# Kernel optimization log

Hardware: AMD Instinct MI355X
Metric: run time of the kernel (lower is better)

The kernel has to match this reference:

```python
import jax, jax.numpy as jnp
import numpy as np

N_USERS, N_ITEMS, D = 16384, 8192, 64
IMG_D, TXT_D = 4096, 384
TOPK = 10
LAMBDA = 0.9         # args.lambda_coeff
NNZ = 786432
N_TOTAL = N_USERS + N_ITEMS


def l2norm(x, eps=1e-12):
    # F.normalize(p=2, dim=1)
    return x / jnp.maximum(jnp.linalg.norm(x, axis=-1, keepdims=True), eps)


def build_knn_graph(feats):
    """build_sim + build_knn_normalized_graph (sparse, sym norm).
    Returns row-sparse KNN graph as (values [N,k], indices [N,k])."""
    z = l2norm(feats)
    sim = z @ z.T                          # [N, N] cosine similarity
    vals, inds = jax.lax.top_k(sim, TOPK)  # [N, k]
    rowsum = vals.sum(axis=1)              # degree
    d_inv_sqrt = jnp.where(rowsum > 0, rowsum, 1.0) ** -0.5
    vals = vals * d_inv_sqrt[:, None] * d_inv_sqrt[inds]  # D^-1/2 A D^-1/2
    return vals, inds


def knn_mm(vals, inds, x):
    # sparse.mm with row-sparse [N,k] graph: out[i] = sum_k vals[i,k]*x[inds[i,k]]
    return jnp.einsum('nk,nkd->nd', vals, x[inds])


def setup_inputs() -> dict:
    key = jax.random.key(0)
    ks = jax.random.split(key, 16)
    xav = lambda k, shp: jax.random.normal(k, shp, jnp.float32) * (2.0 / (shp[0] + shp[-1])) ** 0.5
    return dict(
        adj_rows=jax.random.randint(ks[0], (NNZ,), 0, N_TOTAL, jnp.int32),
        adj_cols=jax.random.randint(ks[1], (NNZ,), 0, N_TOTAL, jnp.int32),
        adj_vals=jax.random.uniform(ks[2], (NNZ,), jnp.float32) / 32.0,
        image_feats=jax.random.normal(ks[3], (N_ITEMS, IMG_D), jnp.float32),
        text_feats=jax.random.normal(ks[4], (N_ITEMS, TXT_D), jnp.float32),
        user_emb=xav(ks[5], (N_USERS, D)),
        item_emb=xav(ks[6], (N_ITEMS, D)),
        img_w=xav(ks[7], (IMG_D, D)), img_b=jnp.zeros((D,), jnp.float32),
        txt_w=xav(ks[8], (TXT_D, D)), txt_b=jnp.zeros((D,), jnp.float32),
        q_w1=xav(ks[9], (D, D)), q_b1=jnp.zeros((D,), jnp.float32),
        q_w2=xav(ks[10], (D, 1)),
        gc_w=xav(ks[11], (2, D, D)), gc_b=jnp.zeros((2, D), jnp.float32),
        bi_w=xav(ks[12], (2, D, D)), bi_b=jnp.zeros((2, D), jnp.float32),
    )


def reference(adj_rows, adj_cols, adj_vals, image_feats, text_feats,
              user_emb, item_emb, img_w, img_b, txt_w, txt_b,
              q_w1, q_b1, q_w2, gc_w, gc_b, bi_w, bi_b):
    # original (init-time) modal graphs from raw features
    io_v, io_i = build_knn_graph(image_feats)
    to_v, to_i = build_knn_graph(text_feats)
    # projected modal features + dynamic graphs (build_item_graph=True)
    img_f = image_feats @ img_w + img_b
    txt_f = text_feats @ txt_w + txt_b
    in_v, in_i = build_knn_graph(img_f)
    tn_v, tn_i = build_knn_graph(txt_f)
    # one propagation layer over (1-l)*new_adj + l*orig_adj (separable for layers=1)
    e = item_emb
    img_e = (1 - LAMBDA) * knn_mm(in_v, in_i, e) + LAMBDA * knn_mm(io_v, io_i, e)
    txt_e = (1 - LAMBDA) * knn_mm(tn_v, tn_i, e) + LAMBDA * knn_mm(to_v, to_i, e)
    # attention-weighted fusion
    query = lambda x: jnp.tanh(x @ q_w1 + q_b1) @ q_w2   # [N_ITEMS, 1]
    att = jnp.concatenate([query(img_e), query(txt_e)], axis=-1)
    w = jax.nn.softmax(att, axis=-1)
    h = w[:, :1] * img_e + w[:, 1:] * txt_e
    # NGCF user-item propagation (dropout p=0 -> identity)
    ego = jnp.concatenate([user_emb, item_emb], axis=0)   # [N_TOTAL, D]
    all_e = [ego]
    for i in range(2):
        side = jax.ops.segment_sum(adj_vals[:, None] * ego[adj_cols], adj_rows,
                                   num_segments=N_TOTAL)
        s = jax.nn.leaky_relu(side @ gc_w[i] + gc_b[i])
        b = jax.nn.leaky_relu((ego * side) @ bi_w[i] + bi_b[i])
        ego = s + b
        all_e.append(l2norm(ego))
    all_e = jnp.mean(jnp.stack(all_e, axis=1), axis=1)
    u_g, i_g = all_e[:N_USERS], all_e[N_USERS:]
    i_g = i_g + l2norm(h)
    return u_g, i_g, img_e, txt_e, h
```

## Files before the change

### kernel.cpp

```cpp
#include <hip/hip_runtime.h>
#include <hip/hip_bf16.h>
#include <math.h>

#define N_USERS 16384
#define N_ITEMS 8192
#define N_TOTAL 24576
#define EMB_D 64
#define IMG_DIM 4096
#define TXT_DIM 384
#define K_TOP 10
#define N_CAND 16
#define NNZ_E 786432

typedef _Float16 f16x8 __attribute__((ext_vector_type(8)));
typedef float f32x4 __attribute__((ext_vector_type(4)));

#define AS1 __attribute__((address_space(1)))
#define AS3 __attribute__((address_space(3)))

__device__ __forceinline__ float leaky01(float x){ return x >= 0.f ? x : 0.01f * x; }

__device__ __forceinline__ void gld16(const void* g, void* l) {
  __builtin_amdgcn_global_load_lds((const AS1 unsigned int*)g, (AS3 unsigned int*)l, 16, 0, 0);
}

__device__ __forceinline__ bool beats(float v, int i, float u, int j) {
  return v > u || (v == u && i < j);
}

__device__ __forceinline__ float h2f(unsigned short u) {
  _Float16 h = __builtin_bit_cast(_Float16, u);
  return (float)h;
}

__global__ __launch_bounds__(256) void norm_cast_fused_k(const float* __restrict__ x,
                                                         float* __restrict__ invn,
                                                         unsigned short* __restrict__ zh, int K) {
  __shared__ __align__(16) float xr[4096];
  __shared__ float red[256];
  int r = blockIdx.x;
  const float* xp = x + (size_t)r * K;
  float ss = 0.f;
  for (int j = threadIdx.x; j < K; j += 256) { float v = xp[j]; xr[j] = v; ss += v * v; }
  red[threadIdx.x] = ss; __syncthreads();
  for (int s = 128; s > 0; s >>= 1) {
    if (threadIdx.x < s) red[threadIdx.x] += red[threadIdx.x + s];
    __syncthreads();
  }
  float inv = 1.f / fmaxf(sqrtf(red[0]), 1e-12f);
  if (threadIdx.x == 0) invn[r] = inv;
  for (int j = threadIdx.x; j < K; j += 256) {
    _Float16 h = (_Float16)(xr[j] * inv);
    zh[(size_t)r * K + j] = __builtin_bit_cast(unsigned short, h);
  }
}

#define EPI_LD 136
__global__ __launch_bounds__(256) void sim_mfma_k(const unsigned short* __restrict__ Zh,
                                                  unsigned short* __restrict__ C, int K, int r0) {
  __shared__ __align__(16) unsigned short smem[128 * EPI_LD];
  unsigned short* smA = smem;
  unsigned short* smB = smem + 128 * 32;
  const int tid = threadIdx.x;
  const int lane = tid & 63;
  const int wid = tid >> 6;
  const int wr = wid >> 1, wc = wid & 1;
  const int bRow = r0 + blockIdx.y * 128;
  const int bCol = blockIdx.x * 128;

  f32x4 acc[4][4];
  const f32x4 fzero = {0.f, 0.f, 0.f, 0.f};
  #pragma unroll
  for (int m = 0; m < 4; m++)
    #pragma unroll
    for (int n = 0; n < 4; n++) acc[m][n] = fzero;

  const int u0 = (wid * 2 + 0) * 64 + lane;
  const int u1 = (wid * 2 + 1) * 64 + lane;
  const int ar0 = u0 >> 2, ac0 = (u0 & 3) * 8;
  const int ar1 = u1 >> 2, ac1 = (u1 & 3) * 8;
  const size_t rowA0 = (size_t)(bRow + ar0) * K;
  const size_t rowA1 = (size_t)(bRow + ar1) * K;
  const size_t rowB0 = (size_t)(bCol + ar0) * K;
  const size_t rowB1 = (size_t)(bCol + ar1) * K;
  unsigned short* ldsA0 = smA + (wid * 2 + 0) * 512;
  unsigned short* ldsA1 = smA + (wid * 2 + 1) * 512;
  unsigned short* ldsB0 = smB + (wid * 2 + 0) * 512;
  unsigned short* ldsB1 = smB + (wid * 2 + 1) * 512;

  const int kc = lane >> 4;
  const int fr = lane & 15;

  for (int k0 = 0; k0 < K; k0 += 32) {
    __syncthreads();
    gld16(Zh + rowA0 + k0 + ac0, ldsA0);
    gld16(Zh + rowA1 + k0 + ac1, ldsA1);
    gld16(Zh + rowB0 + k0 + ac0, ldsB0);
    gld16(Zh + rowB1 + k0 + ac1, ldsB1);
    __syncthreads();

    f16x8 a[4], b[4];
    #pragma unroll
    for (int m = 0; m < 4; m++)
      a[m] = *(const f16x8*)&smA[(wr * 64 + m * 16 + fr) * 32 + kc * 8];
    #pragma unroll
    for (int n = 0; n < 4; n++)
      b[n] = *(const f16x8*)&smB[(wc * 64 + n * 16 + fr) * 32 + kc * 8];
    #pragma unroll
    for (int m = 0; m < 4; m++)
      #pragma unroll
      for (int n = 0; n < 4; n++)
        acc[m][n] = __builtin_amdgcn_mfma_f32_16x16x32_f16(a[m], b[n], acc[m][n], 0, 0, 0);
  }

  __syncthreads();
  const int lr = wr * 64 + (lane >> 4) * 4;
  const int lc = wc * 64 + (lane & 15);
  #pragma unroll
  for (int m = 0; m < 4; m++)
    #pragma unroll
    for (int n = 0; n < 4; n++)
      #pragma unroll
      for (int r = 0; r < 4; r++) {
        _Float16 hv = (_Float16)acc[m][n][r];
        smem[(lr + m * 16 + r) * EPI_LD + lc + n * 16] = __builtin_bit_cast(unsigned short, hv);
      }
  __syncthreads();
  const int outRow0 = blockIdx.y * 128;
  #pragma unroll
  for (int i = 0; i < 8; i++) {
    int idx = i * 2048 + tid * 8;
    int rr = idx >> 7, cc = idx & 127;
    *(uint4*)&C[(size_t)(outRow0 + rr) * N_ITEMS + bCol + cc] =
        *(const uint4*)&smem[rr * EPI_LD + cc];
  }
}

__device__ __forceinline__ void ins4(float val, int idx, float tv[4], int ti[4]) {
  if (beats(val, idx, tv[3], ti[3])) {
    tv[3] = val; ti[3] = idx;
    if (beats(tv[3], ti[3], tv[2], ti[2])) { float a=tv[2];int b=ti[2]; tv[2]=tv[3];ti[2]=ti[3]; tv[3]=a;ti[3]=b; }
    if (beats(tv[2], ti[2], tv[1], ti[1])) { float a=tv[1];int b=ti[1]; tv[1]=tv[2];ti[1]=ti[2]; tv[2]=a;ti[2]=b; }
    if (beats(tv[1], ti[1], tv[0], ti[0])) { float a=tv[0];int b=ti[0]; tv[0]=tv[1];ti[0]=ti[1]; tv[1]=a;ti[1]=b; }
  }
}

__global__ __launch_bounds__(256) void topk16h_k(const unsigned short* __restrict__ sim,
                                                 int r0, int* __restrict__ cand) {
  int row = blockIdx.x * 4 + (threadIdx.x >> 6);
  int lane = threadIdx.x & 63;
  const uint4* s8 = reinterpret_cast<const uint4*>(sim + (size_t)row * N_ITEMS);

  float tv[4]; int ti[4];
  #pragma unroll
  for (int k = 0; k < 4; k++) { tv[k] = -INFINITY; ti[k] = 0x7fffffff; }
  unsigned long long ext0 = 0ull, ext1 = 0ull;

  for (int i = 0; i < 16; i++) {
    uint4 v = s8[i * 64 + lane];
    int base = (i * 64 + lane) * 8;
    ins4(h2f(v.x & 0xffff), base + 0, tv, ti);
    ins4(h2f(v.x >> 16),    base + 1, tv, ti);
    ins4(h2f(v.y & 0xffff), base + 2, tv, ti);
    ins4(h2f(v.y >> 16),    base + 3, tv, ti);
    ins4(h2f(v.z & 0xffff), base + 4, tv, ti);
    ins4(h2f(v.z >> 16),    base + 5, tv, ti);
    ins4(h2f(v.w & 0xffff), base + 6, tv, ti);
    ins4(h2f(v.w >> 16),    base + 7, tv, ti);
  }
  int nvalid = 4;
  for (int t = 0; t < N_CAND; t++) {
    float bv = tv[0]; int bi = ti[0];
    for (int o = 32; o; o >>= 1) {
      float ov = __shfl_xor(bv, o, 64);
      int   oi = __shfl_xor(bi, o, 64);
      if (beats(ov, oi, bv, bi)) { bv = ov; bi = oi; }
    }
    if (tv[0] == bv && ti[0] == bi) {
      int slot = ((bi >> 9) << 3) | (bi & 7);
      if (slot < 64) ext0 |= 1ull << slot; else ext1 |= 1ull << (slot - 64);
      tv[0]=tv[1];ti[0]=ti[1]; tv[1]=tv[2];ti[1]=ti[2]; tv[2]=tv[3];ti[2]=ti[3];
      tv[3]=-INFINITY; ti[3]=0x7fffffff;
      nvalid--;
      if (nvalid == 0) {
        for (int i = 0; i < 16; i++) {
          uint4 v = s8[i * 64 + lane];
          int base = (i * 64 + lane) * 8;
          float vv[8] = {h2f(v.x & 0xffff), h2f(v.x >> 16), h2f(v.y & 0xffff), h2f(v.y >> 16),
                         h2f(v.z & 0xffff), h2f(v.z >> 16), h2f(v.w & 0xffff), h2f(v.w >> 16)};
          #pragma unroll
          for (int q = 0; q < 8; q++) {
            int slot2 = i * 8 + q;
            bool used = (slot2 < 64) ? ((ext0 >> slot2) & 1ull) : ((ext1 >> (slot2 - 64)) & 1ull);
            if (!used) ins4(vv[q], base + q, tv, ti);
          }
        }
        nvalid = 4;
      }
    }
    if (lane == 0) cand[(size_t)(r0 + row) * N_CAND + t] = bi;
  }
}

__global__ __launch_bounds__(256) void refine_k(const float* __restrict__ X, int K,
                                                const float* __restrict__ invn,
                                                const int* __restrict__ cand,
                                                float* __restrict__ vals, int* __restrict__ inds,
                                                float* __restrict__ dis) {
  __shared__ __align__(16) float xr[4096];
  __shared__ float dots[N_CAND];
  int row = blockIdx.x;
  int tid = threadIdx.x, lane = tid & 63, wid = tid >> 6;
  for (int j = tid; j < K; j += 256) xr[j] = X[(size_t)row * K + j];
  __syncthreads();
  for (int c = wid; c < N_CAND; c += 4) {
    int ci = cand[(size_t)row * N_CAND + c];
    const float* xc = X + (size_t)ci * K;
    float p = 0.f;
    if (K == 4096) {
      const float4* xc4 = reinterpret_cast<const float4*>(xc);
      const float4* xr4 = reinterpret_cast<const float4*>(xr);
      for (int it = 0; it < 16; it++) {
        float4 a = xr4[it * 64 + lane];
        float4 g = xc4[it * 64 + lane];
        p += a.x * g.x + a.y * g.y + a.z * g.z + a.w * g.w;
      }
    } else {
      for (int j = lane; j < K; j += 64) p += xr[j] * xc[j];
    }
    for (int o = 32; o; o >>= 1) p += __shfl_xor(p, o, 64);
    if (lane == 0) dots[c] = p;
  }
  __syncthreads();
  if (tid == 0) {
    float v[N_CAND]; int id[N_CAND];
    float ir = invn[row];
    for (int c = 0; c < N_CAND; c++) {
      id[c] = cand[(size_t)row * N_CAND + c];
      v[c] = dots[c] * ir * invn[id[c]];
    }
    for (int a = 1; a < N_CAND; a++) {
      float av = v[a]; int ai = id[a];
      int b = a - 1;
      while (b >= 0 && beats(av, ai, v[b], id[b])) { v[b+1]=v[b]; id[b+1]=id[b]; b--; }
      v[b+1] = av; id[b+1] = ai;
    }
    float sum = 0.f;
    for (int t = 0; t < K_TOP; t++) {
      vals[(size_t)row * K_TOP + t] = v[t];
      inds[(size_t)row * K_TOP + t] = id[t];
      sum += v[t];
    }
    float rs = sum > 0.f ? sum : 1.0f;
    dis[row] = 1.0f / sqrtf(rs);
  }
}

__global__ __launch_bounds__(256) void scale_vals_k(float* __restrict__ vals,
                                                    const int* __restrict__ inds,
                                                    const float* __restrict__ dis, int tot) {
  int idx = blockIdx.x * 256 + threadIdx.x;
  if (idx < tot) {
    int i = idx / K_TOP;
    vals[idx] *= dis[i] * dis[inds[idx]];
  }
}

__global__ __launch_bounds__(256) void linear_splitk_k(const float* __restrict__ X,
                                                       const float* __restrict__ W,
                                                       const float* __restrict__ b,
                                                       float* __restrict__ outp, int K, int KS) {
  __shared__ float As[64][17];
  __shared__ float Ws[16][64];
  int br = blockIdx.x, ks = blockIdx.y;
  int tid = threadIdx.x, tr = tid >> 4, tc = tid & 15;
  int k0 = ks * KS, k1 = k0 + KS;
  int lrow = tid >> 2, lk = (tid & 3) * 4;
  int wrow = tid >> 4, wcol = (tid & 15) * 4;
  float acc[4][4] = {};
  for (int kb = k0; kb < k1; kb += 16) {
    __syncthreads();
    float4 xv = *(const float4*)&X[(size_t)(br * 64 + lrow) * K + kb + lk];
    As[lrow][lk + 0] = xv.x; As[lrow][lk + 1] = xv.y;
    As[lrow][lk + 2] = xv.z; As[lrow][lk + 3] = xv.w;
    *(float4*)&Ws[wrow][wcol] = *(const float4*)&W[(size_t)(kb + wrow) * 64 + wcol];
    __syncthreads();
    #pragma unroll
    for (int k = 0; k < 16; k++) {
      float a[4], w[4];
      #pragma unroll
      for (int i = 0; i < 4; i++) a[i] = As[tr * 4 + i][k];
      #pragma unroll
      for (int j = 0; j < 4; j++) w[j] = Ws[k][tc * 4 + j];
      #pragma unroll
      for (int i = 0; i < 4; i++)
        #pragma unroll
        for (int j = 0; j < 4; j++) acc[i][j] += a[i] * w[j];
    }
  }
  #pragma unroll
  for (int i = 0; i < 4; i++)
    #pragma unroll
    for (int j = 0; j < 4; j++) {
      float v = acc[i][j];
      if (ks == 0) v += b[tc * 4 + j];
      atomicAdd(&outp[(size_t)(br * 64 + tr * 4 + i) * 64 + tc * 4 + j], v);
    }
}

__global__ __launch_bounds__(256) void fuse_knn_k(const float* __restrict__ av, const int* __restrict__ ai,
                                                  const float* __restrict__ bv, const int* __restrict__ bi_,
                                                  const float* __restrict__ e, float* __restrict__ outp,
                                                  float lam) {
  int i = blockIdx.x * 4 + (threadIdx.x >> 6), d = threadIdx.x & 63;
  float sa = 0.f, sb = 0.f;
  #pragma unroll
  for (int k = 0; k < K_TOP; k++) {
    sa += av[(size_t)i * K_TOP + k] * e[(size_t)ai[(size_t)i * K_TOP + k] * 64 + d];
    sb += bv[(size_t)i * K_TOP + k] * e[(size_t)bi_[(size_t)i * K_TOP + k] * 64 + d];
  }
  outp[(size_t)i * 64 + d] = (1.f - lam) * sa + lam * sb;
}

__global__ __launch_bounds__(64) void attn_k(const float* __restrict__ img_e, const float* __restrict__ txt_e,
                                             const float* __restrict__ qw1, const float* __restrict__ qb1,
                                             const float* __restrict__ qw2, float* __restrict__ h) {
  __shared__ float W1[64][64];
  __shared__ float sI[64], sT[64];
  int t = threadIdx.x; int i = blockIdx.x;
  for (int k = 0; k < 64; k++) W1[k][t] = qw1[k * 64 + t];
  sI[t] = img_e[(size_t)i * 64 + t];
  sT[t] = txt_e[(size_t)i * 64 + t];
  __syncthreads();
  float yi = qb1[t], yt = qb1[t];
  #pragma unroll 16
  for (int k = 0; k < 64; k++) { yi += sI[k] * W1[k][t]; yt += sT[k] * W1[k][t]; }
  float w2 = qw2[t];
  float pi = tanhf(yi) * w2, pt = tanhf(yt) * w2;
  for (int o = 32; o > 0; o >>= 1) { pi += __shfl_xor(pi, o, 64); pt += __shfl_xor(pt, o, 64); }
  float m = fmaxf(pi, pt);
  float ei = expf(pi - m), et = expf(pt - m);
  float den = ei + et;
  float w0 = ei / den, w1v = et / den;
  h[(size_t)i * 64 + t] = w0 * sI[t] + w1v * sT[t];
}

__global__ __launch_bounds__(256) void hist_k(const int* __restrict__ rows, int* __restrict__ cnt) {
  int e = blockIdx.x * 256 + threadIdx.x;
  if (e < NNZ_E) atomicAdd(&cnt[rows[e]], 1);
}

__global__ __launch_bounds__(256) void scan_k(const int* __restrict__ cnt,
                                              int* __restrict__ starts,
                                              int* __restrict__ cursor) {
  __shared__ int part[256];
  int t = threadIdx.x;
  int base = t * (N_TOTAL / 256);
  int s = 0;
  for (int j = 0; j < N_TOTAL / 256; j++) s += cnt[base + j];
  part[t] = s;
  __syncthreads();
  for (int off = 1; off < 256; off <<= 1) {
    int v = part[t];
    int u = (t >= off) ? part[t - off] : 0;
    __syncthreads();
    part[t] = v + u;
    __syncthreads();
  }
  int run = (t > 0) ? part[t - 1] : 0;
  for (int j = 0; j < N_TOTAL / 256; j++) {
    starts[base + j] = run;
    cursor[base + j] = run;
    run += cnt[base + j];
  }
  if (t == 255) starts[N_TOTAL] = run;
}

__global__ __launch_bounds__(256) void place_k(const int* __restrict__ rows,
                                               int* __restrict__ cursor, int* __restrict__ perm) {
  int e = blockIdx.x * 256 + threadIdx.x;
  if (e < NNZ_E) {
    int p = atomicAdd(&cursor[rows[e]], 1);
    perm[p] = e;
  }
}

__global__ __launch_bounds__(256) void gather_gcn_k(const int* __restrict__ starts,
                                                    const int* __restrict__ perm,
                                                    const int* __restrict__ cols,
                                                    const float* __restrict__ vals,
                                                    const float* __restrict__ ego,
                                                    float* __restrict__ side) {
  int row = blockIdx.x * 4 + (threadIdx.x >> 6);
  int d = threadIdx.x & 63;
  int s = starts[row], e = starts[row + 1];
  float acc = 0.f;
  for (int i = s; i < e; i++) {
    int eid = perm[i];
    acc += vals[eid] * ego[(size_t)cols[eid] * 64 + d];
  }
  side[(size_t)row * 64 + d] = acc;
}

__global__ __launch_bounds__(256) void gcn_k(const float* __restrict__ side, const float* __restrict__ ego,
                                             const float* __restrict__ gw, const float* __restrict__ gb,
                                             const float* __restrict__ bw, const float* __restrict__ bb,
                                             float* __restrict__ outp) {
  __shared__ float W1[64][64], W2[64][64];
  __shared__ float S[4][64], E[4][64];
  int t = threadIdx.x & 63, rb = threadIdx.x >> 6;
  int r = blockIdx.x * 4 + rb;
  for (int idx = threadIdx.x; idx < 4096; idx += 256) {
    W1[idx >> 6][idx & 63] = gw[idx];
    W2[idx >> 6][idx & 63] = bw[idx];
  }
  S[rb][t] = side[(size_t)r * 64 + t];
  E[rb][t] = ego[(size_t)r * 64 + t];
  __syncthreads();
  float s = gb[t], b = bb[t];
  #pragma unroll 16
  for (int k = 0; k < 64; k++) {
    float sv = S[rb][k];
    s += sv * W1[k][t];
    b += E[rb][k] * sv * W2[k][t];
  }
  outp[(size_t)r * 64 + t] = leaky01(s) + leaky01(b);
}

__global__ __launch_bounds__(256) void l2acc_k(const float* __restrict__ ego, float* __restrict__ acc) {
  int r = blockIdx.x * 4 + (threadIdx.x >> 6), d = threadIdx.x & 63;
  float v = ego[(size_t)r * 64 + d];
  float ss = v * v;
  for (int o = 32; o > 0; o >>= 1) ss += __shfl_xor(ss, o, 64);
  float inv = 1.f / fmaxf(sqrtf(ss), 1e-12f);
  acc[(size_t)r * 64 + d] += v * inv;
}

__global__ __launch_bounds__(256) void init_ego_k(const float* __restrict__ ue, const float* __restrict__ ie,
                                                  float* __restrict__ ego, float* __restrict__ acc) {
  int r = blockIdx.x * 4 + (threadIdx.x >> 6), d = threadIdx.x & 63;
  float v = (r < N_USERS) ? ue[(size_t)r * 64 + d] : ie[(size_t)(r - N_USERS) * 64 + d];
  ego[(size_t)r * 64 + d] = v;
  acc[(size_t)r * 64 + d] = v;
}

__global__ __launch_bounds__(256) void final_k(const float* __restrict__ acc, const float* __restrict__ h,
                                               float* __restrict__ u_g, float* __restrict__ i_g) {
  int r = blockIdx.x * 4 + (threadIdx.x >> 6), d = threadIdx.x & 63;
  float m = acc[(size_t)r * 64 + d] * (1.0f / 3.0f);
  if (r < N_USERS) {
    u_g[(size_t)r * 64 + d] = m;
  } else {
    int i = r - N_USERS;
    float hv = h[(size_t)i * 64 + d];
    float ss = hv * hv;
    for (int o = 32; o > 0; o >>= 1) ss += __shfl_xor(ss, o, 64);
    float inv = 1.f / fmaxf(sqrtf(ss), 1e-12f);
    i_g[(size_t)i * 64 + d] = m + hv * inv;
  }
}

static void build_graph(hipStream_t stream, const float* feats, int K, float* invn,
                        unsigned short* zh, unsigned short* sim, int stripe, int* cand,
                        float* vals, int* inds, float* dis) {
  norm_cast_fused_k<<<N_ITEMS, 256, 0, stream>>>(feats, invn, zh, K);
  for (int r0 = 0; r0 < N_ITEMS; r0 += stripe) {
    int rows = (N_ITEMS - r0) < stripe ? (N_ITEMS - r0) : stripe;
    dim3 g(N_ITEMS / 128, rows / 128);
    sim_mfma_k<<<g, 256, 0, stream>>>(zh, sim, K, r0);
    topk16h_k<<<rows / 4, 256, 0, stream>>>(sim, r0, cand);
  }
  refine_k<<<N_ITEMS, 256, 0, stream>>>(feats, K, invn, cand, vals, inds, dis);
  int tot = N_ITEMS * K_TOP;
  scale_vals_k<<<(tot + 255) / 256, 256, 0, stream>>>(vals, inds, dis, tot);
}

extern "C" void kernel_launch(void* const* d_in, const int* in_sizes, int n_in,
                              void* d_out, int out_size, void* d_ws, size_t ws_size,
                              hipStream_t stream) {
  const int*   adj_rows   = (const int*)d_in[0];
  const int*   adj_cols   = (const int*)d_in[1];
  const float* adj_vals   = (const float*)d_in[2];
  const float* image_feats= (const float*)d_in[3];
  const float* text_feats = (const float*)d_in[4];
  const float* user_emb   = (const float*)d_in[5];
  const float* item_emb   = (const float*)d_in[6];
  const float* img_w      = (const float*)d_in[7];
  const float* img_b      = (const float*)d_in[8];
  const float* txt_w      = (const float*)d_in[9];
  const float* txt_b      = (const float*)d_in[10];
  const float* q_w1       = (const float*)d_in[11];
  const float* q_b1       = (const float*)d_in[12];
  const float* q_w2       = (const float*)d_in[13];
  const float* gc_w       = (const float*)d_in[14];
  const float* gc_b       = (const float*)d_in[15];
  const float* bi_w       = (const float*)d_in[16];
  const float* bi_b       = (const float*)d_in[17];

  float* out  = (float*)d_out;
  float* u_g  = out;
  float* i_g  = u_g + (size_t)N_USERS * 64;
  float* imgE = i_g + (size_t)N_ITEMS * 64;
  float* txtE = imgE + (size_t)N_ITEMS * 64;
  float* hOut = txtE + (size_t)N_ITEMS * 64;

  float* W = (float*)d_ws;
  size_t off = 0;
  auto alloc = [&](size_t n) { float* q = W + off; off += n; return q; };
  float* inv_io = alloc(N_ITEMS);
  float* inv_to = alloc(N_ITEMS);
  float* inv_in = alloc(N_ITEMS);
  float* inv_tn = alloc(N_ITEMS);
  float* img_f  = alloc((size_t)N_ITEMS * 64);
  float* txt_f  = alloc((size_t)N_ITEMS * 64);
  float* vals0 = alloc(N_ITEMS * K_TOP); int* inds0 = (int*)alloc(N_ITEMS * K_TOP);
  float* vals1 = alloc(N_ITEMS * K_TOP); int* inds1 = (int*)alloc(N_ITEMS * K_TOP);
  float* vals2 = alloc(N_ITEMS * K_TOP); int* inds2 = (int*)alloc(N_ITEMS * K_TOP);
  float* vals3 = alloc(N_ITEMS * K_TOP); int* inds3 = (int*)alloc(N_ITEMS * K_TOP);
  float* dis0 = alloc(N_ITEMS);
  float* dis1 = alloc(N_ITEMS);
  float* dis2 = alloc(N_ITEMS);
  float* dis3 = alloc(N_ITEMS);
  int*   cand = (int*)alloc((size_t)N_ITEMS * N_CAND);
  float* ego_a = alloc((size_t)N_TOTAL * 64);
  float* ego_b = alloc((size_t)N_TOTAL * 64);
  float* side  = alloc((size_t)N_TOTAL * 64);
  float* acc   = alloc((size_t)N_TOTAL * 64);
  int* csr_cnt    = (int*)alloc(N_TOTAL);
  int* csr_starts = (int*)alloc(N_TOTAL + 1);
  int* csr_cursor = (int*)alloc(N_TOTAL);
  int* csr_perm   = (int*)alloc(NNZ_E);
  unsigned short* zh = (unsigned short*)alloc(((size_t)N_ITEMS * IMG_DIM) / 2);
  unsigned short* sim = (unsigned short*)(W + off);

  size_t used_bytes = off * 4;
  size_t avail_b = (ws_size > used_bytes) ? (ws_size - used_bytes) : 0;
  long stripe_l = (long)((avail_b / ((size_t)N_ITEMS * 2)) / 128) * 128;
  if (stripe_l > N_ITEMS) stripe_l = N_ITEMS;
  if (stripe_l < 128) stripe_l = 128;
  int stripe = (int)stripe_l;

  hipMemsetAsync(csr_cnt, 0, N_TOTAL * sizeof(int), stream);
  hist_k<<<(NNZ_E + 255) / 256, 256, 0, stream>>>(adj_rows, csr_cnt);
  scan_k<<<1, 256, 0, stream>>>(csr_cnt, csr_starts, csr_cursor);
  place_k<<<(NNZ_E + 255) / 256, 256, 0, stream>>>(adj_rows, csr_cursor, csr_perm);

  build_graph(stream, image_feats, IMG_DIM, inv_io, zh, sim, stripe, cand, vals0, inds0, dis0);
  build_graph(stream, text_feats,  TXT_DIM, inv_to, zh, sim, stripe, cand, vals1, inds1, dis1);

  hipMemsetAsync(img_f, 0, (size_t)N_ITEMS * 64 * sizeof(float), stream);
  hipMemsetAsync(txt_f, 0, (size_t)N_ITEMS * 64 * sizeof(float), stream);
  linear_splitk_k<<<dim3(N_ITEMS / 64, 4), 256, 0, stream>>>(image_feats, img_w, img_b, img_f, IMG_DIM, IMG_DIM / 4);
  linear_splitk_k<<<dim3(N_ITEMS / 64, 4), 256, 0, stream>>>(text_feats,  txt_w, txt_b, txt_f, TXT_DIM, TXT_DIM / 4);

  build_graph(stream, img_f, 64, inv_in, zh, sim, stripe, cand, vals2, inds2, dis2);
  build_graph(stream, txt_f, 64, inv_tn, zh, sim, stripe, cand, vals3, inds3, dis3);

  const float lam = 0.9f;
  fuse_knn_k<<<N_ITEMS / 4, 256, 0, stream>>>(vals2, inds2, vals0, inds0, item_emb, imgE, lam);
  fuse_knn_k<<<N_ITEMS / 4, 256, 0, stream>>>(vals3, inds3, vals1, inds1, item_emb, txtE, lam);

  attn_k<<<N_ITEMS, 64, 0, stream>>>(imgE, txtE, q_w1, q_b1, q_w2, hOut);

  init_ego_k<<<N_TOTAL / 4, 256, 0, stream>>>(user_emb, item_emb, ego_a, acc);

  gather_gcn_k<<<N_TOTAL / 4, 256, 0, stream>>>(csr_starts, csr_perm, adj_cols, adj_vals, ego_a, side);
  gcn_k<<<N_TOTAL / 4, 256, 0, stream>>>(side, ego_a, gc_w, gc_b, bi_w, bi_b, ego_b);
  l2acc_k<<<N_TOTAL / 4, 256, 0, stream>>>(ego_b, acc);

  gather_gcn_k<<<N_TOTAL / 4, 256, 0, stream>>>(csr_starts, csr_perm, adj_cols, adj_vals, ego_b, side);
  gcn_k<<<N_TOTAL / 4, 256, 0, stream>>>(side, ego_b, gc_w + 4096, gc_b + 64, bi_w + 4096, bi_b + 64, ego_a);
  l2acc_k<<<N_TOTAL / 4, 256, 0, stream>>>(ego_a, acc);

  final_k<<<N_TOTAL / 4, 256, 0, stream>>>(acc, hOut, u_g, i_g);
}
```

Baseline: 2.847 ms.

## Exploit similarity symmetry with triangular tiles and store sim matrix in fp32

When the full similarity matrix fits in workspace, the GEMM launches only upper-triangular tiles and writes each off-diagonal tile twice (direct and transposed), which about halves the MFMA work. The sim buffer changes from fp16 to fp32, and top-k reads float4 instead of unpacking halves. In exchange, the sim write and read traffic doubles, the transposed stores are strided and uncoalesced, and a smaller stripe fits in the workspace, which may push execution onto the striped fallback path.

Measured after the change: 2.797 ms. No clear change (-1.8%).

```diff
diff --git a/kernel.cpp b/kernel.cpp
--- a/kernel.cpp
+++ b/kernel.cpp
@@ -11,6 +11,8 @@
 #define K_TOP 10
 #define N_CAND 16
 #define NNZ_E 786432
+#define NTILE 64
+#define TRI_BLOCKS (NTILE * (NTILE + 1) / 2)
 
 typedef _Float16 f16x8 __attribute__((ext_vector_type(8)));
 typedef float f32x4 __attribute__((ext_vector_type(4)));
@@ -26,11 +28,6 @@
 
 __device__ __forceinline__ bool beats(float v, int i, float u, int j) {
   return v > u || (v == u && i < j);
-}
-
-__device__ __forceinline__ float h2f(unsigned short u) {
-  _Float16 h = __builtin_bit_cast(_Float16, u);
-  return (float)h;
 }
 
 __global__ __launch_bounds__(256) void norm_cast_fused_k(const float* __restrict__ x,
@@ -55,18 +52,26 @@
   }
 }
 
-#define EPI_LD 136
 __global__ __launch_bounds__(256) void sim_mfma_k(const unsigned short* __restrict__ Zh,
-                                                  unsigned short* __restrict__ C, int K, int r0) {
-  __shared__ __align__(16) unsigned short smem[128 * EPI_LD];
-  unsigned short* smA = smem;
-  unsigned short* smB = smem + 128 * 32;
+                                                  float* __restrict__ C, int K, int r0, int tri) {
+  __shared__ unsigned short smA[128 * 32];
+  __shared__ unsigned short smB[128 * 32];
   const int tid = threadIdx.x;
   const int lane = tid & 63;
   const int wid = tid >> 6;
   const int wr = wid >> 1, wc = wid & 1;
-  const int bRow = r0 + blockIdx.y * 128;
-  const int bCol = blockIdx.x * 128;
+
+  int tileX, tileY;
+  if (tri) {
+    int b = blockIdx.x, ty = 0, rem = NTILE;
+    while (b >= rem) { b -= rem; ty++; rem--; }
+    tileY = ty; tileX = ty + b;
+  } else {
+    tileX = blockIdx.x; tileY = blockIdx.y;
+  }
+
+  const int bRow = r0 + tileY * 128;
+  const int bCol = tileX * 128;
 
   f32x4 acc[4][4];
   const f32x4 fzero = {0.f, 0.f, 0.f, 0.f};
@@ -113,26 +118,22 @@
         acc[m][n] = __builtin_amdgcn_mfma_f32_16x16x32_f16(a[m], b[n], acc[m][n], 0, 0, 0);
   }
 
-  __syncthreads();
-  const int lr = wr * 64 + (lane >> 4) * 4;
-  const int lc = wc * 64 + (lane & 15);
+  const int crow = tileY * 128 + wr * 64 + (lane >> 4) * 4;
+  const int ccol = bCol + wc * 64 + (lane & 15);
   #pragma unroll
   for (int m = 0; m < 4; m++)
     #pragma unroll
     for (int n = 0; n < 4; n++)
       #pragma unroll
-      for (int r = 0; r < 4; r++) {
-        _Float16 hv = (_Float16)acc[m][n][r];
-        smem[(lr + m * 16 + r) * EPI_LD + lc + n * 16] = __builtin_bit_cast(unsigned short, hv);
-      }
-  __syncthreads();
-  const int outRow0 = blockIdx.y * 128;
-  #pragma unroll
-  for (int i = 0; i < 8; i++) {
-    int idx = i * 2048 + tid * 8;
-    int rr = idx >> 7, cc = idx & 127;
-    *(uint4*)&C[(size_t)(outRow0 + rr) * N_ITEMS + bCol + cc] =
-        *(const uint4*)&smem[rr * EPI_LD + cc];
+      for (int r = 0; r < 4; r++)
+        C[(size_t)(crow + m * 16 + r) * N_ITEMS + ccol + n * 16] = acc[m][n][r];
+
+  if (tri && tileX != tileY) {
+    #pragma unroll
+    for (int m = 0; m < 4; m++)
+      #pragma unroll
+      for (int n = 0; n < 4; n++)
+        *(f32x4*)&C[(size_t)(ccol + n * 16) * N_ITEMS + crow + m * 16] = acc[m][n];
   }
 }
 
@@ -145,28 +146,24 @@
   }
 }
 
-__global__ __launch_bounds__(256) void topk16h_k(const unsigned short* __restrict__ sim,
-                                                 int r0, int* __restrict__ cand) {
+__global__ __launch_bounds__(256) void topk16_k(const float* __restrict__ sim,
+                                                int r0, int* __restrict__ cand) {
   int row = blockIdx.x * 4 + (threadIdx.x >> 6);
   int lane = threadIdx.x & 63;
-  const uint4* s8 = reinterpret_cast<const uint4*>(sim + (size_t)row * N_ITEMS);
+  const float4* s4 = reinterpret_cast<const float4*>(sim + (size_t)row * N_ITEMS);
 
   float tv[4]; int ti[4];
   #pragma unroll
   for (int k = 0; k < 4; k++) { tv[k] = -INFINITY; ti[k] = 0x7fffffff; }
   unsigned long long ext0 = 0ull, ext1 = 0ull;
 
-  for (int i = 0; i < 16; i++) {
-    uint4 v = s8[i * 64 + lane];
-    int base = (i * 64 + lane) * 8;
-    ins4(h2f(v.x & 0xffff), base + 0, tv, ti);
-    ins4(h2f(v.x >> 16),    base + 1, tv, ti);
-    ins4(h2f(v.y & 0xffff), base + 2, tv, ti);
-    ins4(h2f(v.y >> 16),    base + 3, tv, ti);
-    ins4(h2f(v.z & 0xffff), base + 4, tv, ti);
-    ins4(h2f(v.z >> 16),    base + 5, tv, ti);
-    ins4(h2f(v.w & 0xffff), base + 6, tv, ti);
-    ins4(h2f(v.w >> 16),    base + 7, tv, ti);
+  for (int i = 0; i < 32; i++) {
+    float4 v = s4[i * 64 + lane];
+    int base = (i * 64 + lane) * 4;
+    ins4(v.x, base + 0, tv, ti);
+    ins4(v.y, base + 1, tv, ti);
+    ins4(v.z, base + 2, tv, ti);
+    ins4(v.w, base + 3, tv, ti);
   }
   int nvalid = 4;
   for (int t = 0; t < N_CAND; t++) {
@@ -177,20 +174,19 @@
       if (beats(ov, oi, bv, bi)) { bv = ov; bi = oi; }
     }
     if (tv[0] == bv && ti[0] == bi) {
-      int slot = ((bi >> 9) << 3) | (bi & 7);
+      int slot = ((bi >> 8) << 2) | (bi & 3);
       if (slot < 64) ext0 |= 1ull << slot; else ext1 |= 1ull << (slot - 64);
       tv[0]=tv[1];ti[0]=ti[1]; tv[1]=tv[2];ti[1]=ti[2]; tv[2]=tv[3];ti[2]=ti[3];
       tv[3]=-INFINITY; ti[3]=0x7fffffff;
       nvalid--;
       if (nvalid == 0) {
-        for (int i = 0; i < 16; i++) {
-          uint4 v = s8[i * 64 + lane];
-          int base = (i * 64 + lane) * 8;
-          float vv[8] = {h2f(v.x & 0xffff), h2f(v.x >> 16), h2f(v.y & 0xffff), h2f(v.y >> 16),
-                         h2f(v.z & 0xffff), h2f(v.z >> 16), h2f(v.w & 0xffff), h2f(v.w >> 16)};
+        for (int i = 0; i < 32; i++) {
+          float4 v = s4[i * 64 + lane];
+          int base = (i * 64 + lane) * 4;
+          float vv[4] = {v.x, v.y, v.z, v.w};
           #pragma unroll
-          for (int q = 0; q < 8; q++) {
-            int slot2 = i * 8 + q;
+          for (int q = 0; q < 4; q++) {
+            int slot2 = i * 4 + q;
             bool used = (slot2 < 64) ? ((ext0 >> slot2) & 1ull) : ((ext1 >> (slot2 - 64)) & 1ull);
             if (!used) ins4(vv[q], base + q, tv, ti);
           }
@@ -461,14 +457,19 @@
 }
 
 static void build_graph(hipStream_t stream, const float* feats, int K, float* invn,
-                        unsigned short* zh, unsigned short* sim, int stripe, int* cand,
+                        unsigned short* zh, float* sim, int stripe, int* cand,
                         float* vals, int* inds, float* dis) {
   norm_cast_fused_k<<<N_ITEMS, 256, 0, stream>>>(feats, invn, zh, K);
-  for (int r0 = 0; r0 < N_ITEMS; r0 += stripe) {
-    int rows = (N_ITEMS - r0) < stripe ? (N_ITEMS - r0) : stripe;
-    dim3 g(N_ITEMS / 128, rows / 128);
-    sim_mfma_k<<<g, 256, 0, stream>>>(zh, sim, K, r0);
-    topk16h_k<<<rows / 4, 256, 0, stream>>>(sim, r0, cand);
+  if (stripe >= N_ITEMS) {
+    sim_mfma_k<<<TRI_BLOCKS, 256, 0, stream>>>(zh, sim, K, 0, 1);
+    topk16_k<<<N_ITEMS / 4, 256, 0, stream>>>(sim, 0, cand);
+  } else {
+    for (int r0 = 0; r0 < N_ITEMS; r0 += stripe) {
+      int rows = (N_ITEMS - r0) < stripe ? (N_ITEMS - r0) : stripe;
+      dim3 g(N_ITEMS / 128, rows / 128);
+      sim_mfma_k<<<g, 256, 0, stream>>>(zh, sim, K, r0, 0);
+      topk16_k<<<rows / 4, 256, 0, stream>>>(sim, r0, cand);
+    }
   }
   refine_k<<<N_ITEMS, 256, 0, stream>>>(feats, K, invn, cand, vals, inds, dis);
   int tot = N_ITEMS * K_TOP;
@@ -531,11 +532,11 @@
   int* csr_cursor = (int*)alloc(N_TOTAL);
   int* csr_perm   = (int*)alloc(NNZ_E);
   unsigned short* zh = (unsigned short*)alloc(((size_t)N_ITEMS * IMG_DIM) / 2);
-  unsigned short* sim = (unsigned short*)(W + off);
-
-  size_t used_bytes = off * 4;
-  size_t avail_b = (ws_size > used_bytes) ? (ws_size - used_bytes) : 0;
-  long stripe_l = (long)((avail_b / ((size_t)N_ITEMS * 2)) / 128) * 128;
+  float* sim = W + off;
+
+  size_t ws_floats = ws_size / 4;
+  size_t avail = (ws_floats > off) ? (ws_floats - off) : 0;
+  long stripe_l = (long)((avail / N_ITEMS) / 128) * 128;
   if (stripe_l > N_ITEMS) stripe_l = N_ITEMS;
   if (stripe_l < 128) stripe_l = 128;
   int stripe = (int)stripe_l;
```

## Exploit symmetry of similarity matrix by computing upper-triangular tiles only

Applied to the files above, without the earlier changes.

When the whole similarity matrix fits in one stripe, the GEMM launches only upper-triangular 128x128 tiles and writes each tile plus its transpose, roughly halving MFMA work and operand loads. The LDS-staged coalesced epilogue is replaced by direct scattered global stores: 2-byte stores for the normal tile and 8-byte packed stores for the mirrored tile. This trades fewer FLOPs for less coalesced writes, and a serial loop maps block index to tile. The striped path is kept but also uses the uncoalesced epilogue.

New measurement: 2.503 ms. 1.14x faster.

```diff
diff --git a/kernel.cpp b/kernel.cpp
--- a/kernel.cpp
+++ b/kernel.cpp
@@ -11,6 +11,8 @@
 #define K_TOP 10
 #define N_CAND 16
 #define NNZ_E 786432
+#define NTILE 64
+#define TRI_BLOCKS (NTILE * (NTILE + 1) / 2)
 
 typedef _Float16 f16x8 __attribute__((ext_vector_type(8)));
 typedef float f32x4 __attribute__((ext_vector_type(4)));
@@ -31,6 +33,10 @@
 __device__ __forceinline__ float h2f(unsigned short u) {
   _Float16 h = __builtin_bit_cast(_Float16, u);
   return (float)h;
+}
+__device__ __forceinline__ short f2h(float v) {
+  _Float16 h = (_Float16)v;
+  return __builtin_bit_cast(short, h);
 }
 
 __global__ __launch_bounds__(256) void norm_cast_fused_k(const float* __restrict__ x,
@@ -55,18 +61,26 @@
   }
 }
 
-#define EPI_LD 136
 __global__ __launch_bounds__(256) void sim_mfma_k(const unsigned short* __restrict__ Zh,
-                                                  unsigned short* __restrict__ C, int K, int r0) {
-  __shared__ __align__(16) unsigned short smem[128 * EPI_LD];
-  unsigned short* smA = smem;
-  unsigned short* smB = smem + 128 * 32;
+                                                  unsigned short* __restrict__ C, int K, int r0, int tri) {
+  __shared__ unsigned short smA[128 * 32];
+  __shared__ unsigned short smB[128 * 32];
   const int tid = threadIdx.x;
   const int lane = tid & 63;
   const int wid = tid >> 6;
   const int wr = wid >> 1, wc = wid & 1;
-  const int bRow = r0 + blockIdx.y * 128;
-  const int bCol = blockIdx.x * 128;
+
+  int tileX, tileY;
+  if (tri) {
+    int b = blockIdx.x, ty = 0, rem = NTILE;
+    while (b >= rem) { b -= rem; ty++; rem--; }
+    tileY = ty; tileX = ty + b;
+  } else {
+    tileX = blockIdx.x; tileY = blockIdx.y;
+  }
+
+  const int bRow = r0 + tileY * 128;
+  const int bCol = tileX * 128;
 
   f32x4 acc[4][4];
   const f32x4 fzero = {0.f, 0.f, 0.f, 0.f};
@@ -113,26 +127,36 @@
         acc[m][n] = __builtin_amdgcn_mfma_f32_16x16x32_f16(a[m], b[n], acc[m][n], 0, 0, 0);
   }
 
-  __syncthreads();
-  const int lr = wr * 64 + (lane >> 4) * 4;
-  const int lc = wc * 64 + (lane & 15);
-  #pragma unroll
-  for (int m = 0; m < 4; m++)
-    #pragma unroll
-    for (int n = 0; n < 4; n++)
+  const int rloc = wr * 64 + (lane >> 4) * 4;
+  const int cloc = wc * 64 + (lane & 15);
+
+  if (!tri || tileX != tileY) {
+    const int crow = tileY * 128 + rloc;
+    const int ccol = bCol + cloc;
+    #pragma unroll
+    for (int m = 0; m < 4; m++)
       #pragma unroll
-      for (int r = 0; r < 4; r++) {
-        _Float16 hv = (_Float16)acc[m][n][r];
-        smem[(lr + m * 16 + r) * EPI_LD + lc + n * 16] = __builtin_bit_cast(unsigned short, hv);
+      for (int n = 0; n < 4; n++)
+        #pragma unroll
+        for (int r = 0; r < 4; r++)
+          C[(size_t)(crow + m * 16 + r) * N_ITEMS + ccol + n * 16] =
+              (unsigned short)f2h(acc[m][n][r]);
+  }
+
+  if (tri) {
+    #pragma unroll
+    for (int n = 0; n < 4; n++) {
+      const size_t mrow = (size_t)(bCol + cloc + n * 16) * N_ITEMS;
+      #pragma unroll
+      for (int m = 0; m < 4; m++) {
+        short4 pk;
+        pk.x = f2h(acc[m][n][0]);
+        pk.y = f2h(acc[m][n][1]);
+        pk.z = f2h(acc[m][n][2]);
+        pk.w = f2h(acc[m][n][3]);
+        *(short4*)&C[mrow + bRow + rloc + m * 16] = pk;
       }
-  __syncthreads();
-  const int outRow0 = blockIdx.y * 128;
-  #pragma unroll
-  for (int i = 0; i < 8; i++) {
-    int idx = i * 2048 + tid * 8;
-    int rr = idx >> 7, cc = idx & 127;
-    *(uint4*)&C[(size_t)(outRow0 + rr) * N_ITEMS + bCol + cc] =
-        *(const uint4*)&smem[rr * EPI_LD + cc];
+    }
   }
 }
 
@@ -464,11 +488,16 @@
                         unsigned short* zh, unsigned short* sim, int stripe, int* cand,
                         float* vals, int* inds, float* dis) {
   norm_cast_fused_k<<<N_ITEMS, 256, 0, stream>>>(feats, invn, zh, K);
-  for (int r0 = 0; r0 < N_ITEMS; r0 += stripe) {
-    int rows = (N_ITEMS - r0) < stripe ? (N_ITEMS - r0) : stripe;
-    dim3 g(N_ITEMS / 128, rows / 128);
-    sim_mfma_k<<<g, 256, 0, stream>>>(zh, sim, K, r0);
-    topk16h_k<<<rows / 4, 256, 0, stream>>>(sim, r0, cand);
+  if (stripe >= N_ITEMS) {
+    sim_mfma_k<<<TRI_BLOCKS, 256, 0, stream>>>(zh, sim, K, 0, 1);
+    topk16h_k<<<N_ITEMS / 4, 256, 0, stream>>>(sim, 0, cand);
+  } else {
+    for (int r0 = 0; r0 < N_ITEMS; r0 += stripe) {
+      int rows = (N_ITEMS - r0) < stripe ? (N_ITEMS - r0) : stripe;
+      dim3 g(N_ITEMS / 128, rows / 128);
+      sim_mfma_k<<<g, 256, 0, stream>>>(zh, sim, K, r0, 0);
+      topk16h_k<<<rows / 4, 256, 0, stream>>>(sim, r0, cand);
+    }
   }
   refine_k<<<N_ITEMS, 256, 0, stream>>>(feats, K, invn, cand, vals, inds, dis);
   int tot = N_ITEMS * K_TOP;
```
